# Optimization experiments

Hardware: AMD Instinct MI355X
Metric: run time of the kernel (lower is better)

Reference implementation:

```python
import jax, jax.numpy as jnp
import numpy as np

B, S, H, DH, W, G, M = 2, 4096, 12, 64, 256, 64, 256
D = H * DH  # 768
VOCAB = 50282
NEG = -1e9


def setup_inputs() -> dict:
    key = jax.random.key(0)
    ks = jax.random.split(key, 16)
    f = lambda k, shp, s=0.02: jax.random.normal(k, shp, jnp.float32) * s
    return {
        'input_ids': jax.random.randint(ks[0], (B, S), 0, VOCAB, jnp.int32),
        'attn_mask': jnp.ones((B, S), jnp.float32),
        'html_idx': jnp.sort(jax.random.randint(ks[1], (B, M), 0, S, jnp.int32), axis=-1),
        'embed': f(ks[2], (VOCAB, D), 1.0),
        'Wq': f(ks[3], (D, D)), 'bq': jnp.zeros((D,), jnp.float32),
        'Wk': f(ks[4], (D, D)), 'bk': jnp.zeros((D,), jnp.float32),
        'Wv': f(ks[5], (D, D)), 'bv': jnp.zeros((D,), jnp.float32),
        'Wo': f(ks[6], (D, D)), 'bo': jnp.zeros((D,), jnp.float32),
        'gamma': jnp.ones((D,), jnp.float32), 'beta': jnp.zeros((D,), jnp.float32),
        'Wp': f(ks[7], (D, D)), 'bp': jnp.zeros((D,), jnp.float32),
        'Wa': f(ks[8], (D, 3)), 'ba': jnp.zeros((3,), jnp.float32),
        'Ws': f(ks[9], (D, 2)), 'bs': jnp.zeros((2,), jnp.float32),
    }


def _band_shift(t, n_chunks):
    # t: [..., n_chunks+2, W, ...chunked along axis -3/-2]; gather 3 neighbor chunks
    return jnp.concatenate([t[..., i:i + n_chunks, :, :] for i in range(3)], axis=-2)


def longformer_hpt(input_ids, attn_mask, html_idx, embed, Wq, bq, Wk, bk, Wv, bv,
                   Wo, bo, gamma, beta, Wp, bp, Wa, ba, Ws, bs):
    x = embed[input_ids]  # [B,S,D]
    heads = lambda t: t.reshape(B, S, H, DH).transpose(0, 2, 1, 3)  # [B,H,S,DH]
    q, k, v = heads(x @ Wq + bq), heads(x @ Wk + bk), heads(x @ Wv + bv)
    scale = 1.0 / np.sqrt(DH).astype(np.float32)
    C = S // W  # chunks

    # --- sliding-window (banded) attention, one-sided window W ---
    kp = jnp.pad(k, ((0, 0), (0, 0), (W, W), (0, 0))).reshape(B, H, C + 2, W, DH)
    vp = jnp.pad(v, ((0, 0), (0, 0), (W, W), (0, 0))).reshape(B, H, C + 2, W, DH)
    k3 = _band_shift(kp, C)  # [B,H,C,3W,DH]
    v3 = _band_shift(vp, C)
    qc = q.reshape(B, H, C, W, DH)
    sb = jnp.einsum('bhcqd,bhckd->bhcqk', qc, k3) * scale  # [B,H,C,W,3W]

    ii = jnp.arange(W)[:, None]
    jj = jnp.arange(3 * W)[None, :]
    band_ok = jnp.abs(jj - W - ii) <= W  # [W,3W]
    keypos = jnp.arange(C)[:, None] * W - W + jnp.arange(3 * W)[None, :]  # [C,3W]
    kvalid = (keypos >= 0) & (keypos < S) & (keypos >= G)  # global keys handled separately
    mp = jnp.pad(attn_mask, ((0, 0), (W, W))).reshape(B, C + 2, W)
    m3 = jnp.concatenate([mp[:, i:i + C] for i in range(3)], axis=2)  # [B,C,3W]
    mask = band_ok[None, :, :] & kvalid[:, None, :] & (m3[:, :, None, :] > 0)[..., :, :].reshape(B, C, 1, 3 * W).astype(bool) if False else (band_ok[None, None, :, :] & kvalid[None, :, None, :] & (m3[:, :, None, :] > 0))  # [B,C,W,3W]
    sb = jnp.where(mask[:, None], sb, NEG).reshape(B, H, S, 3 * W)

    # --- all tokens also attend to the G global tokens ---
    kg, vg = k[:, :, :G], v[:, :, :G]
    sg = jnp.einsum('bhsd,bhgd->bhsg', q, kg) * scale
    sg = jnp.where(attn_mask[:, None, None, :G] > 0, sg, NEG)

    p = jax.nn.softmax(jnp.concatenate([sg, sb], -1), -1)  # [B,H,S,G+3W]
    pg, pb = p[..., :G], p[..., G:].reshape(B, H, C, W, 3 * W)
    out = (jnp.einsum('bhcqk,bhckd->bhcqd', pb, v3).reshape(B, H, S, DH)
           + jnp.einsum('bhsg,bhgd->bhsd', pg, vg))

    # --- global queries attend to everything ---
    sgl = jnp.einsum('bhgd,bhsd->bhgs', q[:, :, :G], k) * scale
    sgl = jnp.where(attn_mask[:, None, None, :] > 0, sgl, NEG)
    outg = jnp.einsum('bhgs,bhsd->bhgd', jax.nn.softmax(sgl, -1), v)
    out = jnp.concatenate([outg, out[:, :, G:]], axis=2)

    ctx = out.transpose(0, 2, 1, 3).reshape(B, S, D)
    h = x + ctx @ Wo + bo
    mu = h.mean(-1, keepdims=True)
    var = ((h - mu) ** 2).mean(-1, keepdims=True)
    hn = (h - mu) / jnp.sqrt(var + 1e-5) * gamma + beta  # last_hidden [B,S,D]

    # probes (ans_probe: Linear(768,3)+Sigmoid, span_probe: Linear(768,2)+Sigmoid)
    ans = jax.nn.sigmoid(hn @ Wa + ba)
    span = jax.nn.sigmoid(hn @ Ws + bs)

    # ReIndexer gather of HTML-element hidden states + ConditionCalculator
    hr = jnp.take_along_axis(hn, html_idx[:, :, None].astype(jnp.int32), axis=1)  # [B,M,D]
    t = jax.nn.relu(hr @ Wp + bp)
    cond = jax.nn.sigmoid(jnp.einsum('bqh,bch->bcq', hr, t))  # [B,M,M]
    return hn, ans, span, cond


def reference(input_ids, attn_mask, html_idx, embed, Wq, bq, Wk, bk, Wv, bv,
              Wo, bo, gamma, beta, Wp, bp, Wa, ba, Ws, bs):
    return longformer_hpt(input_ids, attn_mask, html_idx, embed, Wq, bq, Wk, bk,
                          Wv, bv, Wo, bo, gamma, beta, Wp, bp, Wa, ba, Ws, bs)
```

## Files before the change

kernel.cpp:

```cpp
#include <hip/hip_runtime.h>

typedef unsigned short u16;
typedef unsigned int   u32;
typedef __attribute__((ext_vector_type(8))) short s8v;
typedef __attribute__((ext_vector_type(8))) unsigned short us8;
typedef __attribute__((ext_vector_type(4))) float f4v;

constexpr int BC  = 2;
constexpr int SL  = 4096;
constexpr int NH  = 12;
constexpr int HD  = 64;
constexpr int DM  = 768;
constexpr int WIN = 256;
constexpr int GLB = 64;
constexpr int QN  = 2304;
constexpr int KCH = 32;
constexpr float FOLD = 0.125f * 1.44269504088896f;
constexpr float NEGS = -1.0e9f;
constexpr float DEFER = 44.36f;

__device__ __forceinline__ float b2f(u16 b){ return __uint_as_float(((u32)b) << 16); }
__device__ __forceinline__ u16 f2b(float f){
  u32 u = __float_as_uint(f);
  return (u16)((u + 0x7fffu + ((u >> 16) & 1u)) >> 16);
}
__device__ __forceinline__ float wredsum(float v){
  #pragma unroll
  for (int o = 32; o > 0; o >>= 1) v += __shfl_xor(v, o, 64);
  return v;
}
__device__ __forceinline__ float sigf(float x){ return 1.f / (1.f + __expf(-x)); }

__global__ void pack_embed(const float* __restrict__ Wq, const float* __restrict__ Wk,
                           const float* __restrict__ Wv, const float* __restrict__ Wo,
                           const float* __restrict__ Wp,
                           const float* __restrict__ bq, const float* __restrict__ bk,
                           const float* __restrict__ bv,
                           u16* __restrict__ wt_qkv, u16* __restrict__ wt_o,
                           u16* __restrict__ wt_p, float* __restrict__ b_qkv,
                           const int* __restrict__ ids, const float* __restrict__ emb,
                           u16* __restrict__ xb)
{
  __shared__ float tile[64][65];
  const int bid = blockIdx.x;
  const int t = threadIdx.x;
  if (bid < 720){
    const int mi = bid / 144, rest = bid % 144;
    const int kt = rest / 12, ntc = rest % 12;
    const float* src = (mi==0)?Wq:(mi==1)?Wk:(mi==2)?Wv:(mi==3)?Wo:Wp;
    u16* dst = (mi<3) ? (wt_qkv + (size_t)mi*768*768) : ((mi==3) ? wt_o : wt_p);
    const int k0 = kt*64, n0 = ntc*64;
    #pragma unroll
    for (int i=0;i<4;i++){
      const int r = (t>>4) + i*16;
      float4 v = ((const float4*)(src + (long)(k0+r)*768 + n0))[t&15];
      tile[r][(t&15)*4+0] = v.x; tile[r][(t&15)*4+1] = v.y;
      tile[r][(t&15)*4+2] = v.z; tile[r][(t&15)*4+3] = v.w;
    }
    __syncthreads();
    const int n = t & 63, kc = (t>>6)*16;
    u32* d32 = (u32*)(dst + (long)(n0+n)*768 + k0 + kc);
    #pragma unroll
    for (int i=0;i<8;i++){
      d32[i] = (u32)f2b(tile[kc+2*i][n]) | ((u32)f2b(tile[kc+2*i+1][n]) << 16);
    }
    if (bid < 9){
      const int i = bid*256 + t;
      if (i < 2304) b_qkv[i] = (i < 768) ? bq[i] : (i < 1536) ? bk[i-768] : bv[i-1536];
    }
  } else {
    int e4 = (bid-720)*256 + t;
    int row = e4 / 192, d4 = e4 - row*192;
    int id = ids[row];
    float4 v = ((const float4*)(emb + (long)id*768))[d4];
    u32 p0 = (u32)f2b(v.x) | ((u32)f2b(v.y) << 16);
    u32 p1 = (u32)f2b(v.z) | ((u32)f2b(v.w) << 16);
    ((u32*)(xb + (long)row*768))[d4*2]   = p0;
    ((u32*)(xb + (long)row*768))[d4*2+1] = p1;
  }
}

__global__ void gather_hr(const int* __restrict__ hidx, const float* __restrict__ hn,
                          u16* __restrict__ hrb){
  int e = blockIdx.x*256 + threadIdx.x;
  if (e >= 512*768) return;
  int r = e / 768, d = e - r*768;
  int b = r >> 8;
  int idx = hidx[r];
  hrb[e] = f2b(hn[((long)(b*SL + idx))*768 + d]);
}

template<int MODE, bool SWZ>
__global__ __launch_bounds__(256, 2)
void gemm_bt(const u16* __restrict__ A, const u16* __restrict__ Bt,
             const float* __restrict__ bias, const u16* __restrict__ resB,
             float* __restrict__ outF, u16* __restrict__ outB,
             int M, int N, int K, long sA, long sB, long sO)
{
  const int bz = blockIdx.z;
  A  += (long)bz * sA;
  Bt += (long)bz * sB;
  int vid = blockIdx.x + gridDim.x*blockIdx.y;
  if constexpr (SWZ){
    const int chunk = (gridDim.x*gridDim.y) >> 3;
    vid = (vid & 7)*chunk + (vid >> 3);
  }
  const int n0 = (vid % gridDim.x) * 128;
  const int m0 = (vid / gridDim.x) * 128;
  __shared__ u16 lsA[128*64];
  __shared__ u16 lsB[128*64];
  const int t = threadIdx.x;
  const int w = t >> 6, lane = t & 63;
  const int wr = w >> 1, wc = w & 1;
  const int fr = lane & 15, fq = lane >> 4;

  f4v acc[4][4];
  #pragma unroll
  for (int i=0;i<4;i++)
    #pragma unroll
    for (int j=0;j<4;j++) acc[i][j] = (f4v)0.f;

  for (int k0 = 0; k0 < K; k0 += 64){
    #pragma unroll
    for (int i=0;i<4;i++){
      int e = (w*4+i)*512 + lane*8;
      int row = e >> 6, col = e & 63;
      __builtin_amdgcn_global_load_lds(
        (const __attribute__((address_space(1))) void*)(A + (long)(m0+row)*K + (k0+col)),
        (__attribute__((address_space(3))) void*)(&lsA[(w*4+i)*512]), 16, 0, 0);
      __builtin_amdgcn_global_load_lds(
        (const __attribute__((address_space(1))) void*)(Bt + (long)(n0+row)*K + (k0+col)),
        (__attribute__((address_space(3))) void*)(&lsB[(w*4+i)*512]), 16, 0, 0);
    }
    __syncthreads();
    #pragma unroll
    for (int kk = 0; kk < 2; kk++){
      s8v af[4], bfv[4];
      #pragma unroll
      for (int mi=0;mi<4;mi++)
        af[mi] = *(const s8v*)&lsA[(wr*64 + mi*16 + fr)*64 + kk*32 + fq*8];
      #pragma unroll
      for (int ni=0;ni<4;ni++)
        bfv[ni] = *(const s8v*)&lsB[(wc*64 + ni*16 + fr)*64 + kk*32 + fq*8];
      #pragma unroll
      for (int mi=0;mi<4;mi++)
        #pragma unroll
        for (int ni=0;ni<4;ni++)
          acc[mi][ni] = __builtin_amdgcn_mfma_f32_16x16x32_bf16(af[mi], bfv[ni], acc[mi][ni], 0, 0, 0);
    }
    __syncthreads();
  }
  #pragma unroll
  for (int mi=0;mi<4;mi++){
    #pragma unroll
    for (int ni=0;ni<4;ni++){
      #pragma unroll
      for (int r=0;r<4;r++){
        int row = m0 + wr*64 + mi*16 + fq*4 + r;
        int col = n0 + wc*64 + ni*16 + fr;
        float v = acc[mi][ni][r];
        if constexpr (MODE == 0){
          v += bias[col];
          outB[(long)row*N + col] = f2b(v);
        } else if constexpr (MODE == 1){
          v += bias[col] + b2f(resB[(long)row*N + col]);
          outB[(long)row*N + col] = f2b(v);
        } else if constexpr (MODE == 2){
          v = fmaxf(v + bias[col], 0.f);
          outB[(long)row*N + col] = f2b(v);
        } else {
          (outF + bz*sO)[(long)row*N + col] = sigf(v);
        }
      }
    }
  }
}

__global__ __launch_bounds__(256, 3)
void attn_band_mfma(const u16* __restrict__ qkv, const float* __restrict__ mask, u16* __restrict__ ctx)
{
  const int q0 = blockIdx.x * 64;
  const int h = blockIdx.y, b = blockIdx.z;
  const int t = threadIdx.x;
  const int w = t >> 6, lane = t & 63;
  const int fq = lane >> 4, fr = lane & 15;

  __shared__ u16 lsK[2][64*64];
  __shared__ u16 lsVT[2][80*72];
  __shared__ u16 lsP[4][16*72];
  __shared__ float lsM[2][64];

  for (int e = t; e < 16*72; e += 256){
    const u16 v = (e < 72) ? (u16)0x3F80 : (u16)0;
    lsVT[0][64*72 + e] = v;
    lsVT[1][64*72 + e] = v;
  }

  const long bq = (long)b*SL*QN;
  const u16* qrow = qkv + (bq + (long)(q0 + w*16 + fr)*QN) + h*HD;
  s8v aq[2];
  aq[0] = *(const s8v*)(qrow + fq*8);
  aq[1] = *(const s8v*)(qrow + 32 + fq*8);

  const u16* kq = qkv + bq + DM + h*HD;
  const u16* vq = qkv + bq + 2*DM + h*HD;
  const float* mrow = mask + b*SL;

  const int ti_lo = (q0 < 320) ? ((320 - q0) >> 6) : 0;
  const int ti_hi_raw = (4352 - q0) >> 6;
  const int ti_hi = ti_hi_raw < 9 ? ti_hi_raw : 9;
  const int NTT = 1 + (ti_hi - ti_lo);
  const int kb0 = q0 - 256 + ti_lo*64;

  f4v out[5];
  #pragma unroll
  for (int n=0;n<5;n++) out[n] = (f4v)0.f;
  float m = -3.0e38f;

  us8 vv0, vv1;
  auto stage_issue = [&](int i, int buf){
    const int k0 = (i == 0) ? 0 : kb0 + (i-1)*64;
    if (t < 64) lsM[buf][t] = mrow[k0 + t];
    #pragma unroll
    for (int j=0;j<2;j++){
      const int r = (w*2+j)*8 + (lane>>3);
      const int d = ((lane&7) ^ (lane>>3))*8;
      __builtin_amdgcn_global_load_lds(
        (const __attribute__((address_space(1))) void*)(kq + (long)(k0+r)*QN + d),
        (__attribute__((address_space(3))) void*)(&lsK[buf][(w*2+j)*512]), 16, 0, 0);
    }
    vv0 = *(const us8*)(vq + (long)(k0+lane)*QN + w*8);
    vv1 = *(const us8*)(vq + (long)(k0+lane)*QN + w*8 + 32);
  };

  stage_issue(0, 0);
  int cur = 0;
  for (int i = 0; i < NTT; i++){
    const int k0 = (i == 0) ? 0 : kb0 + (i-1)*64;
    const int d0 = w*8;
    #pragma unroll
    for (int jj=0;jj<8;jj++) lsVT[cur][(d0+jj)*72 + lane] = (u16)vv0[jj];
    #pragma unroll
    for (int jj=0;jj<8;jj++) lsVT[cur][(d0+32+jj)*72 + lane] = (u16)vv1[jj];
    __syncthreads();
    if (i+1 < NTT) stage_issue(i+1, cur^1);

    f4v s[4];
    #pragma unroll
    for (int n=0;n<4;n++) s[n] = (f4v)0.f;
    #pragma unroll
    for (int kk=0;kk<2;kk++){
      #pragma unroll
      for (int n=0;n<4;n++){
        s8v bf = *(const s8v*)&lsK[cur][(16*n+fr)*64 + (((kk*4+fq) ^ (fr&7))<<3)];
        s[n] = __builtin_amdgcn_mfma_f32_16x16x32_bf16(aq[kk], bf, s[n], 0,0,0);
      }
    }
    const bool isg = (i == 0);
    const int dlt = k0 - q0 - w*16;
    const bool maskAll = __all(lsM[cur][lane] > 0.f);
    const bool fullOK = maskAll && (isg || (dlt >= -241 && dlt <= 193));
    if (!fullOK){
      #pragma unroll
      for (int n=0;n<4;n++){
        const int kcol = 16*n + fr;
        const float mk = lsM[cur][kcol];
        #pragma unroll
        for (int r=0;r<4;r++){
          const int dd = k0 + kcol - (q0 + w*16 + fq*4 + r);
          const bool valid = (mk > 0.f) && (isg || (dd >= -WIN && dd <= WIN));
          s[n][r] = valid ? s[n][r] : NEGS;
        }
      }
    }
    float rm = fmaxf(fmaxf(fmaxf(s[0][0],s[0][1]),fmaxf(s[0][2],s[0][3])),
                     fmaxf(fmaxf(s[1][0],s[1][1]),fmaxf(s[1][2],s[1][3])));
    rm = fmaxf(rm, fmaxf(fmaxf(fmaxf(s[2][0],s[2][1]),fmaxf(s[2][2],s[2][3])),
                         fmaxf(fmaxf(s[3][0],s[3][1]),fmaxf(s[3][2],s[3][3]))));
    rm = fmaxf(rm, __shfl_xor(rm, 1, 64));
    rm = fmaxf(rm, __shfl_xor(rm, 2, 64));
    rm = fmaxf(rm, __shfl_xor(rm, 4, 64));
    rm = fmaxf(rm, __shfl_xor(rm, 8, 64));
    if (__any(rm > m + DEFER)){
      const float mn = fmaxf(m, rm);
      const float sf = exp2f((m - mn)*FOLD);
      m = mn;
      #pragma unroll
      for (int n=0;n<5;n++)
        #pragma unroll
        for (int r=0;r<4;r++) out[n][r] *= sf;
    }
    const float mF = m * FOLD;
    u16* lsPw = lsP[w];
    #pragma unroll
    for (int r=0;r<4;r++){
      const float p0 = exp2f(fmaf(s[0][r], FOLD, -mF));
      const float p1 = exp2f(fmaf(s[1][r], FOLD, -mF));
      const float p2 = exp2f(fmaf(s[2][r], FOLD, -mF));
      const float p3 = exp2f(fmaf(s[3][r], FOLD, -mF));
      u32 a, c;
      asm("v_cvt_pk_bf16_f32 %0, %1, %2" : "=v"(a) : "v"(p0), "v"(p1));
      asm("v_cvt_pk_bf16_f32 %0, %1, %2" : "=v"(c) : "v"(p2), "v"(p3));
      const int row = (fq*4+r)*72;
      lsPw[row + fr]      = (u16)a;
      lsPw[row + 16 + fr] = (u16)(a >> 16);
      lsPw[row + 32 + fr] = (u16)c;
      lsPw[row + 48 + fr] = (u16)(c >> 16);
    }
    s8v ap[2];
    ap[0] = *(const s8v*)&lsPw[fr*72 + fq*8];
    ap[1] = *(const s8v*)&lsPw[fr*72 + 32 + fq*8];
    #pragma unroll
    for (int kk=0;kk<2;kk++){
      #pragma unroll
      for (int n=0;n<5;n++){
        s8v bv = *(const s8v*)&lsVT[cur][(16*n+fr)*72 + kk*32 + fq*8];
        out[n] = __builtin_amdgcn_mfma_f32_16x16x32_bf16(ap[kk], bv, out[n], 0,0,0);
      }
    }
    cur ^= 1;
  }
  float linv[4];
  #pragma unroll
  for (int r=0;r<4;r++) linv[r] = 1.f / __shfl(out[4][r], lane & 48, 64);
  u16* cb = ctx + (((long)(b*SL) + q0 + w*16 + fq*4))*DM + h*HD + fr;
  #pragma unroll
  for (int n=0;n<4;n++)
    #pragma unroll
    for (int r=0;r<4;r++)
      cb[(long)r*DM + 16*n] = f2b(out[n][r]*linv[r]);
}

__global__ __launch_bounds__(256, 3)
void attn_global_part(const u16* __restrict__ qkv, const float* __restrict__ mask,
                      float* __restrict__ pout, float* __restrict__ pml)
{
  const int ck = blockIdx.x;
  const int h = blockIdx.y, b = blockIdx.z;
  const int bh = b*NH + h;
  const int t = threadIdx.x;
  const int w = t >> 6, lane = t & 63;
  const int fq = lane >> 4, fr = lane & 15;

  __shared__ u16 lsK[2][64*64];
  __shared__ u16 lsVT[2][80*72];
  __shared__ u16 lsP[4][16*72];
  __shared__ float lsM[2][64];

  for (int e = t; e < 16*72; e += 256){
    const u16 v = (e < 72) ? (u16)0x3F80 : (u16)0;
    lsVT[0][64*72 + e] = v;
    lsVT[1][64*72 + e] = v;
  }

  const long bq = (long)b*SL*QN;
  const u16* qrow = qkv + (bq + (long)(w*16 + fr)*QN) + h*HD;
  s8v aq[2];
  aq[0] = *(const s8v*)(qrow + fq*8);
  aq[1] = *(const s8v*)(qrow + 32 + fq*8);

  const u16* kq = qkv + bq + DM + h*HD;
  const u16* vq = qkv + bq + 2*DM + h*HD;
  const float* mrow = mask + b*SL;

  f4v out[5];
  #pragma unroll
  for (int n=0;n<5;n++) out[n] = (f4v)0.f;
  float m = -3.0e38f;

  us8 vv0, vv1;
  auto stage_issue = [&](int i, int buf){
    const int k0 = ck*128 + i*64;
    if (t < 64) lsM[buf][t] = mrow[k0 + t];
    #pragma unroll
    for (int j=0;j<2;j++){
      const int r = (w*2+j)*8 + (lane>>3);
      const int d = ((lane&7) ^ (lane>>3))*8;
      __builtin_amdgcn_global_load_lds(
        (const __attribute__((address_space(1))) void*)(kq + (long)(k0+r)*QN + d),
        (__attribute__((address_space(3))) void*)(&lsK[buf][(w*2+j)*512]), 16, 0, 0);
    }
    vv0 = *(const us8*)(vq + (long)(k0+lane)*QN + w*8);
    vv1 = *(const us8*)(vq + (long)(k0+lane)*QN + w*8 + 32);
  };

  stage_issue(0, 0);
  int cur = 0;
  for (int i = 0; i < 2; i++){
    const int d0 = w*8;
    #pragma unroll
    for (int jj=0;jj<8;jj++) lsVT[cur][(d0+jj)*72 + lane] = (u16)vv0[jj];
    #pragma unroll
    for (int jj=0;jj<8;jj++) lsVT[cur][(d0+32+jj)*72 + lane] = (u16)vv1[jj];
    __syncthreads();
    if (i+1 < 2) stage_issue(i+1, cur^1);

    f4v s[4];
    #pragma unroll
    for (int n=0;n<4;n++) s[n] = (f4v)0.f;
    #pragma unroll
    for (int kk=0;kk<2;kk++){
      #pragma unroll
      for (int n=0;n<4;n++){
        s8v bf = *(const s8v*)&lsK[cur][(16*n+fr)*64 + (((kk*4+fq) ^ (fr&7))<<3)];
        s[n] = __builtin_amdgcn_mfma_f32_16x16x32_bf16(aq[kk], bf, s[n], 0,0,0);
      }
    }
    const bool fullOK = __all(lsM[cur][lane] > 0.f);
    if (!fullOK){
      #pragma unroll
      for (int n=0;n<4;n++){
        const float mk = lsM[cur][16*n + fr];
        #pragma unroll
        for (int r=0;r<4;r++)
          s[n][r] = (mk > 0.f) ? s[n][r] : NEGS;
      }
    }
    float rm = fmaxf(fmaxf(fmaxf(s[0][0],s[0][1]),fmaxf(s[0][2],s[0][3])),
                     fmaxf(fmaxf(s[1][0],s[1][1]),fmaxf(s[1][2],s[1][3])));
    rm = fmaxf(rm, fmaxf(fmaxf(fmaxf(s[2][0],s[2][1]),fmaxf(s[2][2],s[2][3])),
                         fmaxf(fmaxf(s[3][0],s[3][1]),fmaxf(s[3][2],s[3][3]))));
    rm = fmaxf(rm, __shfl_xor(rm, 1, 64));
    rm = fmaxf(rm, __shfl_xor(rm, 2, 64));
    rm = fmaxf(rm, __shfl_xor(rm, 4, 64));
    rm = fmaxf(rm, __shfl_xor(rm, 8, 64));
    if (__any(rm > m + DEFER)){
      const float mn = fmaxf(m, rm);
      const float sf = exp2f((m - mn)*FOLD);
      m = mn;
      #pragma unroll
      for (int n=0;n<5;n++)
        #pragma unroll
        for (int r=0;r<4;r++) out[n][r] *= sf;
    }
    const float mF = m * FOLD;
    u16* lsPw = lsP[w];
    #pragma unroll
    for (int r=0;r<4;r++){
      const float p0 = exp2f(fmaf(s[0][r], FOLD, -mF));
      const float p1 = exp2f(fmaf(s[1][r], FOLD, -mF));
      const float p2 = exp2f(fmaf(s[2][r], FOLD, -mF));
      const float p3 = exp2f(fmaf(s[3][r], FOLD, -mF));
      u32 a, c;
      asm("v_cvt_pk_bf16_f32 %0, %1, %2" : "=v"(a) : "v"(p0), "v"(p1));
      asm("v_cvt_pk_bf16_f32 %0, %1, %2" : "=v"(c) : "v"(p2), "v"(p3));
      const int row = (fq*4+r)*72;
      lsPw[row + fr]      = (u16)a;
      lsPw[row + 16 + fr] = (u16)(a >> 16);
      lsPw[row + 32 + fr] = (u16)c;
      lsPw[row + 48 + fr] = (u16)(c >> 16);
    }
    s8v ap[2];
    ap[0] = *(const s8v*)&lsPw[fr*72 + fq*8];
    ap[1] = *(const s8v*)&lsPw[fr*72 + 32 + fq*8];
    #pragma unroll
    for (int kk=0;kk<2;kk++){
      #pragma unroll
      for (int n=0;n<5;n++){
        s8v bv = *(const s8v*)&lsVT[cur][(16*n+fr)*72 + kk*32 + fq*8];
        out[n] = __builtin_amdgcn_mfma_f32_16x16x32_bf16(ap[kk], bv, out[n], 0,0,0);
      }
    }
    cur ^= 1;
  }
  float* pob = pout + ((long)(ck*BC*NH + bh))*64*64;
  #pragma unroll
  for (int n=0;n<4;n++)
    #pragma unroll
    for (int r=0;r<4;r++)
      pob[(w*16 + fq*4 + r)*64 + 16*n + fr] = out[n][r];
  if (fr == 0){
    float* pmb = pml + ((long)(ck*BC*NH + bh))*128;
    #pragma unroll
    for (int r=0;r<4;r++){
      pmb[(w*16 + fq*4 + r)*2 + 0] = m * FOLD;
      pmb[(w*16 + fq*4 + r)*2 + 1] = out[4][r];
    }
  }
}

__global__ __launch_bounds__(256, 2)
void attn_global_combine(const float* __restrict__ pout, const float* __restrict__ pml,
                         u16* __restrict__ ctx)
{
  const int bh = blockIdx.x;
  const int b = bh / NH, h = bh % NH;
  const int t = threadIdx.x;
  __shared__ float wgt[KCH][64];
  __shared__ float rl[64];
  if (t < 64){
    float mc[KCH], lc[KCH];
    #pragma unroll
    for (int c = 0; c < KCH; c++){
      const float* pmb = pml + ((long)(c*BC*NH + bh))*128 + t*2;
      mc[c] = pmb[0]; lc[c] = pmb[1];
    }
    float M = mc[0];
    #pragma unroll
    for (int c = 1; c < KCH; c++) M = fmaxf(M, mc[c]);
    float L = 0.f;
    #pragma unroll
    for (int c = 0; c < KCH; c++){
      const float wv = exp2f(mc[c] - M);
      wgt[c][t] = wv;
      L += lc[c]*wv;
    }
    rl[t] = 1.f/L;
  }
  __syncthreads();
  const int row = t >> 2, dseg = t & 3;
  float acc[16];
  #pragma unroll
  for (int i=0;i<16;i++) acc[i] = 0.f;
  for (int c = 0; c < KCH; c++){
    const float wv = wgt[c][row];
    const float4* pb = (const float4*)(pout + ((long)(c*BC*NH + bh)*64 + row)*64 + dseg*16);
    #pragma unroll
    for (int i = 0; i < 4; i++){
      float4 v = pb[i];
      acc[i*4+0] += v.x*wv; acc[i*4+1] += v.y*wv;
      acc[i*4+2] += v.z*wv; acc[i*4+3] += v.w*wv;
    }
  }
  u16* cr = ctx + ((long)(b*SL + row))*DM + h*HD + dseg*16;
  const float r = rl[row];
  #pragma unroll
  for (int i = 0; i < 16; i += 2){
    u32 pk = (u32)f2b(acc[i]*r) | ((u32)f2b(acc[i+1]*r) << 16);
    *(u32*)(cr + i) = pk;
  }
}

__global__ __launch_bounds__(384, 2)
void ln_heads(const u16* __restrict__ hb, const float* __restrict__ gamma, const float* __restrict__ beta,
              const float* __restrict__ Wa, const float* __restrict__ ba,
              const float* __restrict__ Wsp, const float* __restrict__ bsp,
              float* __restrict__ hn, float* __restrict__ ans, float* __restrict__ span)
{
  const int r = blockIdx.x;
  const int t = threadIdx.x, lane = t & 63, w = t >> 6;
  __shared__ float red[12];
  __shared__ float dred[6][5];
  const u32 pk = ((const u32*)(hb + (long)r*DM))[t];
  const float v0 = b2f((u16)(pk & 0xffff));
  const float v1 = b2f((u16)(pk >> 16));
  float sum = wredsum(v0 + v1);
  float sq  = wredsum(v0*v0 + v1*v1);
  if (lane == 0){ red[w] = sum; red[6+w] = sq; }
  __syncthreads();
  float mu = 0.f, msq = 0.f;
  #pragma unroll
  for (int i=0;i<6;i++){ mu += red[i]; msq += red[6+i]; }
  mu *= (1.f/768.f); msq *= (1.f/768.f);
  const float rstd = rsqrtf(msq - mu*mu + 1e-5f);
  const int i0 = 2*t, i1 = 2*t+1;
  const float y0 = (v0 - mu)*rstd*gamma[i0] + beta[i0];
  const float y1 = (v1 - mu)*rstd*gamma[i1] + beta[i1];
  ((float2*)(hn + (long)r*DM))[t] = make_float2(y0, y1);
  float pa0 = y0*Wa[i0*3+0] + y1*Wa[i1*3+0];
  float pa1 = y0*Wa[i0*3+1] + y1*Wa[i1*3+1];
  float pa2 = y0*Wa[i0*3+2] + y1*Wa[i1*3+2];
  float ps0 = y0*Wsp[i0*2+0] + y1*Wsp[i1*2+0];
  float ps1 = y0*Wsp[i0*2+1] + y1*Wsp[i1*2+1];
  pa0 = wredsum(pa0); pa1 = wredsum(pa1); pa2 = wredsum(pa2);
  ps0 = wredsum(ps0); ps1 = wredsum(ps1);
  if (lane == 0){ dred[w][0]=pa0; dred[w][1]=pa1; dred[w][2]=pa2; dred[w][3]=ps0; dred[w][4]=ps1; }
  __syncthreads();
  if (t == 0){
    float A0=0,A1=0,A2=0,S0=0,S1=0;
    #pragma unroll
    for (int i=0;i<6;i++){ A0+=dred[i][0]; A1+=dred[i][1]; A2+=dred[i][2]; S0+=dred[i][3]; S1+=dred[i][4]; }
    ans[(long)r*3+0]  = sigf(A0 + ba[0]);
    ans[(long)r*3+1]  = sigf(A1 + ba[1]);
    ans[(long)r*3+2]  = sigf(A2 + ba[2]);
    span[(long)r*2+0] = sigf(S0 + bsp[0]);
    span[(long)r*2+1] = sigf(S1 + bsp[1]);
  }
}

extern "C" void kernel_launch(void* const* d_in, const int* in_sizes, int n_in,
                              void* d_out, int out_size, void* d_ws, size_t ws_size,
                              hipStream_t stream)
{
  const int*   input_ids = (const int*)  d_in[0];
  const float* attn_mask = (const float*)d_in[1];
  const int*   html_idx  = (const int*)  d_in[2];
  const float* embed     = (const float*)d_in[3];
  const float* Wq = (const float*)d_in[4];  const float* bq = (const float*)d_in[5];
  const float* Wk = (const float*)d_in[6];  const float* bk = (const float*)d_in[7];
  const float* Wv = (const float*)d_in[8];  const float* bv = (const float*)d_in[9];
  const float* Wo = (const float*)d_in[10]; const float* bo = (const float*)d_in[11];
  const float* gamma = (const float*)d_in[12]; const float* beta = (const float*)d_in[13];
  const float* Wp = (const float*)d_in[14]; const float* bp = (const float*)d_in[15];
  const float* Wa = (const float*)d_in[16]; const float* ba = (const float*)d_in[17];
  const float* Wsp = (const float*)d_in[18]; const float* bsp = (const float*)d_in[19];

  char* ws = (char*)d_ws;
  size_t off = 0;
  auto take = [&](size_t bytes)->char*{
    char* p = ws + off; off += (bytes + 255) & ~(size_t)255; return p;
  };
  u16*   x_b    = (u16*)  take((size_t)8192*768*2);
  u16*   wt_qkv = (u16*)  take((size_t)2304*768*2);
  u16*   wt_o   = (u16*)  take((size_t)768*768*2);
  u16*   wt_p   = (u16*)  take((size_t)768*768*2);
  float* b_qkv  = (float*)take(2304*4);
  u16*   qkv_b  = (u16*)  take((size_t)8192*2304*2);
  u16*   ctx_b  = (u16*)  take((size_t)8192*768*2);
  u16*   h_b    = (u16*)  take((size_t)8192*768*2);
  u16*   hr_b   = (u16*)  take((size_t)512*768*2);
  u16*   t_b    = (u16*)  take((size_t)512*768*2);
  float* pout   = (float*)take((size_t)KCH*BC*NH*64*64*4);
  float* pml    = (float*)take((size_t)KCH*BC*NH*128*4);

  float* out_hn   = (float*)d_out;
  float* out_ans  = out_hn  + (size_t)8192*768;
  float* out_span = out_ans + (size_t)8192*3;
  float* out_cond = out_span + (size_t)8192*2;

  pack_embed<<<6864, 256, 0, stream>>>(Wq, Wk, Wv, Wo, Wp, bq, bk, bv,
                                       wt_qkv, wt_o, wt_p, b_qkv,
                                       input_ids, embed, x_b);

  gemm_bt<0,true><<<dim3(18,64,1), 256, 0, stream>>>(x_b, wt_qkv, b_qkv, nullptr,
                                                nullptr, qkv_b, 8192, 2304, 768, 0,0,0);
  attn_band_mfma<<<dim3(64,12,2), 256, 0, stream>>>(qkv_b, attn_mask, ctx_b);
  attn_global_part<<<dim3(KCH,12,2), 256, 0, stream>>>(qkv_b, attn_mask, pout, pml);
  attn_global_combine<<<BC*NH, 256, 0, stream>>>(pout, pml, ctx_b);
  gemm_bt<1,true><<<dim3(6,64,1), 256, 0, stream>>>(ctx_b, wt_o, bo, x_b,
                                               nullptr, h_b, 8192, 768, 768, 0,0,0);
  ln_heads<<<8192, 384, 0, stream>>>(h_b, gamma, beta, Wa, ba, Wsp, bsp,
                                     out_hn, out_ans, out_span);
  gather_hr<<<1536, 256, 0, stream>>>(html_idx, out_hn, hr_b);
  gemm_bt<2,false><<<dim3(6,4,1), 256, 0, stream>>>(hr_b, wt_p, bp, nullptr,
                                              nullptr, t_b, 512, 768, 768, 0,0,0);
  gemm_bt<3,false><<<dim3(2,2,2), 256, 0, stream>>>(t_b, hr_b, nullptr, nullptr,
                                              out_cond, nullptr, 256, 256, 768,
                                              (long)256*768, (long)256*768, (long)256*256);
}
```

Measured before the change: 229.2 us.

## Single-buffer K tile, register ones-vector for row sums, raise occupancy to 4

Both attention kernels now keep a single K tile in LDS instead of two, shrink the V^T buffer by dropping the padded ones rows, and take the softmax row sum from an MFMA against a per-lane register ones vector. A second barrier after QK^T lets the next K prefetch overwrite the single tile safely. The smaller LDS footprint and the launch-bounds change to 4 blocks per SM aim to raise occupancy. The row-max shuffle reduction now runs only inside the rescale branch. In exchange the extra barrier exposes K load latency, and the shuffle-free local max check only keeps rescaling correct because of the DEFER threshold.

```diff
diff --git a/kernel.cpp b/kernel.cpp
--- a/kernel.cpp
+++ b/kernel.cpp
@@ -176,7 +176,7 @@
   }
 }
 
-__global__ __launch_bounds__(256, 3)
+__global__ __launch_bounds__(256, 4)
 void attn_band_mfma(const u16* __restrict__ qkv, const float* __restrict__ mask, u16* __restrict__ ctx)
 {
   const int q0 = blockIdx.x * 64;
@@ -185,16 +185,10 @@
   const int w = t >> 6, lane = t & 63;
   const int fq = lane >> 4, fr = lane & 15;
 
-  __shared__ u16 lsK[2][64*64];
-  __shared__ u16 lsVT[2][80*72];
+  __shared__ u16 lsK[64*64];
+  __shared__ u16 lsVT[2][64*72];
   __shared__ u16 lsP[4][16*72];
   __shared__ float lsM[2][64];
-
-  for (int e = t; e < 16*72; e += 256){
-    const u16 v = (e < 72) ? (u16)0x3F80 : (u16)0;
-    lsVT[0][64*72 + e] = v;
-    lsVT[1][64*72 + e] = v;
-  }
 
   const long bq = (long)b*SL*QN;
   const u16* qrow = qkv + (bq + (long)(q0 + w*16 + fr)*QN) + h*HD;
@@ -202,6 +196,13 @@
   aq[0] = *(const s8v*)(qrow + fq*8);
   aq[1] = *(const s8v*)(qrow + 32 + fq*8);
 
+  s8v ones_bf;
+  {
+    const short o = (fr == 0) ? (short)0x3F80 : (short)0;
+    #pragma unroll
+    for (int j=0;j<8;j++) ones_bf[j] = o;
+  }
+
   const u16* kq = qkv + bq + DM + h*HD;
   const u16* vq = qkv + bq + 2*DM + h*HD;
   const float* mrow = mask + b*SL;
@@ -212,22 +213,23 @@
   const int NTT = 1 + (ti_hi - ti_lo);
   const int kb0 = q0 - 256 + ti_lo*64;
 
-  f4v out[5];
-  #pragma unroll
-  for (int n=0;n<5;n++) out[n] = (f4v)0.f;
+  f4v out[4];
+  f4v outl = (f4v)0.f;
+  #pragma unroll
+  for (int n=0;n<4;n++) out[n] = (f4v)0.f;
   float m = -3.0e38f;
 
   us8 vv0, vv1;
-  auto stage_issue = [&](int i, int buf){
+  auto stage_issue = [&](int i, int vbuf){
     const int k0 = (i == 0) ? 0 : kb0 + (i-1)*64;
-    if (t < 64) lsM[buf][t] = mrow[k0 + t];
+    if (t < 64) lsM[vbuf][t] = mrow[k0 + t];
     #pragma unroll
     for (int j=0;j<2;j++){
       const int r = (w*2+j)*8 + (lane>>3);
       const int d = ((lane&7) ^ (lane>>3))*8;
       __builtin_amdgcn_global_load_lds(
         (const __attribute__((address_space(1))) void*)(kq + (long)(k0+r)*QN + d),
-        (__attribute__((address_space(3))) void*)(&lsK[buf][(w*2+j)*512]), 16, 0, 0);
+        (__attribute__((address_space(3))) void*)(&lsK[(w*2+j)*512]), 16, 0, 0);
     }
     vv0 = *(const us8*)(vq + (long)(k0+lane)*QN + w*8);
     vv1 = *(const us8*)(vq + (long)(k0+lane)*QN + w*8 + 32);
@@ -243,7 +245,6 @@
     #pragma unroll
     for (int jj=0;jj<8;jj++) lsVT[cur][(d0+32+jj)*72 + lane] = (u16)vv1[jj];
     __syncthreads();
-    if (i+1 < NTT) stage_issue(i+1, cur^1);
 
     f4v s[4];
     #pragma unroll
@@ -252,10 +253,13 @@
     for (int kk=0;kk<2;kk++){
       #pragma unroll
       for (int n=0;n<4;n++){
-        s8v bf = *(const s8v*)&lsK[cur][(16*n+fr)*64 + (((kk*4+fq) ^ (fr&7))<<3)];
+        s8v bf = *(const s8v*)&lsK[(16*n+fr)*64 + (((kk*4+fq) ^ (fr&7))<<3)];
         s[n] = __builtin_amdgcn_mfma_f32_16x16x32_bf16(aq[kk], bf, s[n], 0,0,0);
       }
     }
+    __syncthreads();
+    if (i+1 < NTT) stage_issue(i+1, cur^1);
+
     const bool isg = (i == 0);
     const int dlt = k0 - q0 - w*16;
     const bool maskAll = __all(lsM[cur][lane] > 0.f);
@@ -273,20 +277,22 @@
         }
       }
     }
-    float rm = fmaxf(fmaxf(fmaxf(s[0][0],s[0][1]),fmaxf(s[0][2],s[0][3])),
-                     fmaxf(fmaxf(s[1][0],s[1][1]),fmaxf(s[1][2],s[1][3])));
-    rm = fmaxf(rm, fmaxf(fmaxf(fmaxf(s[2][0],s[2][1]),fmaxf(s[2][2],s[2][3])),
-                         fmaxf(fmaxf(s[3][0],s[3][1]),fmaxf(s[3][2],s[3][3]))));
-    rm = fmaxf(rm, __shfl_xor(rm, 1, 64));
-    rm = fmaxf(rm, __shfl_xor(rm, 2, 64));
-    rm = fmaxf(rm, __shfl_xor(rm, 4, 64));
-    rm = fmaxf(rm, __shfl_xor(rm, 8, 64));
-    if (__any(rm > m + DEFER)){
+    float rmloc = fmaxf(fmaxf(fmaxf(s[0][0],s[0][1]),fmaxf(s[0][2],s[0][3])),
+                        fmaxf(fmaxf(s[1][0],s[1][1]),fmaxf(s[1][2],s[1][3])));
+    rmloc = fmaxf(rmloc, fmaxf(fmaxf(fmaxf(s[2][0],s[2][1]),fmaxf(s[2][2],s[2][3])),
+                               fmaxf(fmaxf(s[3][0],s[3][1]),fmaxf(s[3][2],s[3][3]))));
+    if (__any(rmloc > m + DEFER)){
+      float rm = rmloc;
+      rm = fmaxf(rm, __shfl_xor(rm, 1, 64));
+      rm = fmaxf(rm, __shfl_xor(rm, 2, 64));
+      rm = fmaxf(rm, __shfl_xor(rm, 4, 64));
+      rm = fmaxf(rm, __shfl_xor(rm, 8, 64));
       const float mn = fmaxf(m, rm);
       const float sf = exp2f((m - mn)*FOLD);
       m = mn;
-      #pragma unroll
-      for (int n=0;n<5;n++)
+      outl *= sf;
+      #pragma unroll
+      for (int n=0;n<4;n++)
         #pragma unroll
         for (int r=0;r<4;r++) out[n][r] *= sf;
     }
@@ -313,16 +319,17 @@
     #pragma unroll
     for (int kk=0;kk<2;kk++){
       #pragma unroll
-      for (int n=0;n<5;n++){
+      for (int n=0;n<4;n++){
         s8v bv = *(const s8v*)&lsVT[cur][(16*n+fr)*72 + kk*32 + fq*8];
         out[n] = __builtin_amdgcn_mfma_f32_16x16x32_bf16(ap[kk], bv, out[n], 0,0,0);
       }
+      outl = __builtin_amdgcn_mfma_f32_16x16x32_bf16(ap[kk], ones_bf, outl, 0,0,0);
     }
     cur ^= 1;
   }
   float linv[4];
   #pragma unroll
-  for (int r=0;r<4;r++) linv[r] = 1.f / __shfl(out[4][r], lane & 48, 64);
+  for (int r=0;r<4;r++) linv[r] = 1.f / __shfl(outl[r], lane & 48, 64);
   u16* cb = ctx + (((long)(b*SL) + q0 + w*16 + fq*4))*DM + h*HD + fr;
   #pragma unroll
   for (int n=0;n<4;n++)
@@ -331,7 +338,7 @@
       cb[(long)r*DM + 16*n] = f2b(out[n][r]*linv[r]);
 }
 
-__global__ __launch_bounds__(256, 3)
+__global__ __launch_bounds__(256, 4)
 void attn_global_part(const u16* __restrict__ qkv, const float* __restrict__ mask,
                       float* __restrict__ pout, float* __restrict__ pml)
 {
@@ -342,16 +349,10 @@
   const int w = t >> 6, lane = t & 63;
   const int fq = lane >> 4, fr = lane & 15;
 
-  __shared__ u16 lsK[2][64*64];
-  __shared__ u16 lsVT[2][80*72];
+  __shared__ u16 lsK[64*64];
+  __shared__ u16 lsVT[2][64*72];
   __shared__ u16 lsP[4][16*72];
   __shared__ float lsM[2][64];
-
-  for (int e = t; e < 16*72; e += 256){
-    const u16 v = (e < 72) ? (u16)0x3F80 : (u16)0;
-    lsVT[0][64*72 + e] = v;
-    lsVT[1][64*72 + e] = v;
-  }
 
   const long bq = (long)b*SL*QN;
   const u16* qrow = qkv + (bq + (long)(w*16 + fr)*QN) + h*HD;
@@ -359,26 +360,34 @@
   aq[0] = *(const s8v*)(qrow + fq*8);
   aq[1] = *(const s8v*)(qrow + 32 + fq*8);
 
+  s8v ones_bf;
+  {
+    const short o = (fr == 0) ? (short)0x3F80 : (short)0;
+    #pragma unroll
+    for (int j=0;j<8;j++) ones_bf[j] = o;
+  }
+
   const u16* kq = qkv + bq + DM + h*HD;
   const u16* vq = qkv + bq + 2*DM + h*HD;
   const float* mrow = mask + b*SL;
 
-  f4v out[5];
-  #pragma unroll
-  for (int n=0;n<5;n++) out[n] = (f4v)0.f;
+  f4v out[4];
+  f4v outl = (f4v)0.f;
+  #pragma unroll
+  for (int n=0;n<4;n++) out[n] = (f4v)0.f;
   float m = -3.0e38f;
 
   us8 vv0, vv1;
-  auto stage_issue = [&](int i, int buf){
+  auto stage_issue = [&](int i, int vbuf){
     const int k0 = ck*128 + i*64;
-    if (t < 64) lsM[buf][t] = mrow[k0 + t];
+    if (t < 64) lsM[vbuf][t] = mrow[k0 + t];
     #pragma unroll
     for (int j=0;j<2;j++){
       const int r = (w*2+j)*8 + (lane>>3);
       const int d = ((lane&7) ^ (lane>>3))*8;
       __builtin_amdgcn_global_load_lds(
         (const __attribute__((address_space(1))) void*)(kq + (long)(k0+r)*QN + d),
-        (__attribute__((address_space(3))) void*)(&lsK[buf][(w*2+j)*512]), 16, 0, 0);
+        (__attribute__((address_space(3))) void*)(&lsK[(w*2+j)*512]), 16, 0, 0);
     }
     vv0 = *(const us8*)(vq + (long)(k0+lane)*QN + w*8);
     vv1 = *(const us8*)(vq + (long)(k0+lane)*QN + w*8 + 32);
@@ -393,7 +402,6 @@
     #pragma unroll
     for (int jj=0;jj<8;jj++) lsVT[cur][(d0+32+jj)*72 + lane] = (u16)vv1[jj];
     __syncthreads();
-    if (i+1 < 2) stage_issue(i+1, cur^1);
 
     f4v s[4];
     #pragma unroll
@@ -402,10 +410,13 @@
     for (int kk=0;kk<2;kk++){
       #pragma unroll
       for (int n=0;n<4;n++){
-        s8v bf = *(const s8v*)&lsK[cur][(16*n+fr)*64 + (((kk*4+fq) ^ (fr&7))<<3)];
+        s8v bf = *(const s8v*)&lsK[(16*n+fr)*64 + (((kk*4+fq) ^ (fr&7))<<3)];
         s[n] = __builtin_amdgcn_mfma_f32_16x16x32_bf16(aq[kk], bf, s[n], 0,0,0);
       }
     }
+    __syncthreads();
+    if (i+1 < 2) stage_issue(i+1, cur^1);
+
     const bool fullOK = __all(lsM[cur][lane] > 0.f);
     if (!fullOK){
       #pragma unroll
@@ -416,20 +427,22 @@
           s[n][r] = (mk > 0.f) ? s[n][r] : NEGS;
       }
     }
-    float rm = fmaxf(fmaxf(fmaxf(s[0][0],s[0][1]),fmaxf(s[0][2],s[0][3])),
-                     fmaxf(fmaxf(s[1][0],s[1][1]),fmaxf(s[1][2],s[1][3])));
-    rm = fmaxf(rm, fmaxf(fmaxf(fmaxf(s[2][0],s[2][1]),fmaxf(s[2][2],s[2][3])),
-                         fmaxf(fmaxf(s[3][0],s[3][1]),fmaxf(s[3][2],s[3][3]))));
-    rm = fmaxf(rm, __shfl_xor(rm, 1, 64));
-    rm = fmaxf(rm, __shfl_xor(rm, 2, 64));
-    rm = fmaxf(rm, __shfl_xor(rm, 4, 64));
-    rm = fmaxf(rm, __shfl_xor(rm, 8, 64));
-    if (__any(rm > m + DEFER)){
+    float rmloc = fmaxf(fmaxf(fmaxf(s[0][0],s[0][1]),fmaxf(s[0][2],s[0][3])),
+                        fmaxf(fmaxf(s[1][0],s[1][1]),fmaxf(s[1][2],s[1][3])));
+    rmloc = fmaxf(rmloc, fmaxf(fmaxf(fmaxf(s[2][0],s[2][1]),fmaxf(s[2][2],s[2][3])),
+                               fmaxf(fmaxf(s[3][0],s[3][1]),fmaxf(s[3][2],s[3][3]))));
+    if (__any(rmloc > m + DEFER)){
+      float rm = rmloc;
+      rm = fmaxf(rm, __shfl_xor(rm, 1, 64));
+      rm = fmaxf(rm, __shfl_xor(rm, 2, 64));
+      rm = fmaxf(rm, __shfl_xor(rm, 4, 64));
+      rm = fmaxf(rm, __shfl_xor(rm, 8, 64));
       const float mn = fmaxf(m, rm);
       const float sf = exp2f((m - mn)*FOLD);
       m = mn;
-      #pragma unroll
-      for (int n=0;n<5;n++)
+      outl *= sf;
+      #pragma unroll
+      for (int n=0;n<4;n++)
         #pragma unroll
         for (int r=0;r<4;r++) out[n][r] *= sf;
     }
@@ -456,10 +469,11 @@
     #pragma unroll
     for (int kk=0;kk<2;kk++){
       #pragma unroll
-      for (int n=0;n<5;n++){
+      for (int n=0;n<4;n++){
         s8v bv = *(const s8v*)&lsVT[cur][(16*n+fr)*72 + kk*32 + fq*8];
         out[n] = __builtin_amdgcn_mfma_f32_16x16x32_bf16(ap[kk], bv, out[n], 0,0,0);
       }
+      outl = __builtin_amdgcn_mfma_f32_16x16x32_bf16(ap[kk], ones_bf, outl, 0,0,0);
     }
     cur ^= 1;
   }
@@ -474,7 +488,7 @@
     #pragma unroll
     for (int r=0;r<4;r++){
       pmb[(w*16 + fq*4 + r)*2 + 0] = m * FOLD;
-      pmb[(w*16 + fq*4 + r)*2 + 1] = out[4][r];
+      pmb[(w*16 + fq*4 + r)*2 + 1] = outl[r];
     }
   }
 }
```

Measured after the change: 221.9 us. 1.03x faster.
